# Kernel tuning notes

Hardware: AMD Instinct MI355X
Metric: run time of the kernel (lower is better)

Reference implementation:

```python
import jax, jax.numpy as jnp
import numpy as np

D_MODEL = 1024
HEADS = 16
HEAD_DIM = D_MODEL // HEADS


def setup_inputs() -> dict:
    key = jax.random.key(0)
    ks = jax.random.split(key, 9)
    s = 1.0 / np.sqrt(D_MODEL)
    inp = {
        "inputs": jax.random.normal(ks[0], (4, 2048, D_MODEL), dtype=jnp.float32),
        "Wq": jax.random.normal(ks[1], (D_MODEL, D_MODEL), dtype=jnp.float32) * s,
        "bq": jnp.zeros((D_MODEL,), dtype=jnp.float32),
        "Wk": jax.random.normal(ks[2], (D_MODEL, D_MODEL), dtype=jnp.float32) * s,
        "bk": jnp.zeros((D_MODEL,), dtype=jnp.float32),
        "Wv": jax.random.normal(ks[3], (D_MODEL, D_MODEL), dtype=jnp.float32) * s,
        "bv": jnp.zeros((D_MODEL,), dtype=jnp.float32),
        "Wo": jax.random.normal(ks[4], (D_MODEL, D_MODEL), dtype=jnp.float32) * s,
        "bo": jnp.zeros((D_MODEL,), dtype=jnp.float32),
    }
    return inp


def reference(inputs, Wq, bq, Wk, bk, Wv, bv, Wo, bo):
    bs, seq, _ = inputs.shape
    # projections -> [b, h, s, d]
    def split_heads(x):
        return x.reshape(bs, seq, HEADS, HEAD_DIM).transpose(0, 2, 1, 3)
    q = split_heads(inputs @ Wq + bq)
    k = split_heads(inputs @ Wk + bk)
    v = split_heads(inputs @ Wv + bv)
    # NOTE: original code divides by (head_dim ** 1 / 2) == head_dim/2, not sqrt(head_dim)
    scale = HEAD_DIM / 2.0
    scores = jnp.einsum("bhqd,bhkd->bhqk", q, k) / scale
    attn = jax.nn.softmax(scores, axis=-1)
    out = jnp.einsum("bhqk,bhkd->bhqd", attn, v)
    out = out.transpose(0, 2, 1, 3).reshape(bs, seq, HEADS * HEAD_DIM)
    return out @ Wo + bo
```

## Files before the change

kernel.cpp:

```cpp
#include <hip/hip_runtime.h>
#include <stdint.h>

typedef __attribute__((ext_vector_type(8))) short bf16x8;
typedef __attribute__((ext_vector_type(4))) float f32x4;
typedef __attribute__((address_space(1))) void as1_void;
typedef __attribute__((address_space(3))) void as3_void;

#define D_MODEL 1024
#define SEQ     2048
#define BATCH   4
#define HEADS   16
#define HDIM    64

#define QSCALE 0.045084220029218407f

__device__ __forceinline__ ushort f2bf(float f) {
  union { float f; unsigned u; } v; v.f = f;
  unsigned u = v.u + 0x7fffu + ((v.u >> 16) & 1u);
  return (ushort)(u >> 16);
}

__device__ __forceinline__ void gload_lds16(const void* g, void* l) {
  __builtin_amdgcn_global_load_lds((as1_void*)(uintptr_t)g, (as3_void*)l, 16, 0, 0);
}

__device__ __forceinline__ bf16x8 pack8(float a0, float a1, float a2, float a3,
                                        float a4, float a5, float a6, float a7) {
  union { uint u[4]; bf16x8 v; } x;
  x.u[0] = __builtin_amdgcn_perm(__float_as_uint(a1), __float_as_uint(a0), 0x07060302);
  x.u[1] = __builtin_amdgcn_perm(__float_as_uint(a3), __float_as_uint(a2), 0x07060302);
  x.u[2] = __builtin_amdgcn_perm(__float_as_uint(a5), __float_as_uint(a4), 0x07060302);
  x.u[3] = __builtin_amdgcn_perm(__float_as_uint(a7), __float_as_uint(a6), 0x07060302);
  return x.v;
}

__global__ void prep_kernel(const float* __restrict__ X,
                            const float* w0, const float* w1, const float* w2, const float* w3,
                            const float* __restrict__ bq, const float* __restrict__ bk,
                            const float* __restrict__ bv,
                            ushort* __restrict__ Xb, ushort* __restrict__ WT,
                            float* __restrict__ bcat) {
  __shared__ float tile[32][33];
  const int bx = blockIdx.x, t = threadIdx.x;
  if (bx < 8192) {
    int i = bx * 256 + t;
    float4 f = reinterpret_cast<const float4*>(X)[i];
    ushort4 o;
    o.x = f2bf(f.x); o.y = f2bf(f.y); o.z = f2bf(f.z); o.w = f2bf(f.w);
    reinterpret_cast<ushort4*>(Xb)[i] = o;
  } else if (bx < 12288) {
    int tz = bx - 8192;
    int z = tz >> 10;
    int xy = tz & 1023;
    int bxt = xy & 31, byt = xy >> 5;
    const float* w = (z == 0) ? w0 : (z == 1) ? w1 : (z == 2) ? w2 : w3;
    const float sc = (z == 0) ? QSCALE : 1.0f;
    ushort* o = WT + (size_t)z * D_MODEL * D_MODEL;
    int tx = t & 31, ty = t >> 5;
    int x = bxt * 32 + tx;
    int y0 = byt * 32;
    #pragma unroll
    for (int i = ty; i < 32; i += 8)
      tile[i][tx] = w[(size_t)(y0 + i) * D_MODEL + x];
    __syncthreads();
    #pragma unroll
    for (int i = ty; i < 32; i += 8)
      o[(size_t)(bxt * 32 + i) * D_MODEL + y0 + tx] = f2bf(tile[tx][i] * sc);
  } else {
    int i = (bx - 12288) * 256 + t;
    bcat[i] = (i < 1024) ? bq[i] * QSCALE : (i < 2048) ? bk[i - 1024] : bv[i - 2048];
  }
}

__global__ __launch_bounds__(256) void gemm_qkv(const ushort* __restrict__ A, const ushort* __restrict__ BT,
                                                const float* __restrict__ bias,
                                                ushort* __restrict__ QK, ushort* __restrict__ Vt) {
  __shared__ __align__(16) ushort As[128 * 32];
  __shared__ __align__(16) ushort Bs[128 * 32];
  const int K = D_MODEL;
  const int tid  = threadIdx.x;
  const int w    = tid >> 6;
  const int lane = tid & 63;
  const int lo   = lane & 15, quad = lane >> 4;
  const int m0 = blockIdx.y * 128, n0 = blockIdx.x * 128;
  const int ra = lane >> 2;
  const int ca = (lane & 3) * 8;
  const int wm = (w & 1) * 64, wn = (w >> 1) * 64;

  f32x4 acc[4][4];
  #pragma unroll
  for (int i = 0; i < 4; ++i)
    #pragma unroll
    for (int j = 0; j < 4; ++j) acc[i][j] = {0.f, 0.f, 0.f, 0.f};

  for (int k0 = 0; k0 < K; k0 += 32) {
    #pragma unroll
    for (int i = 0; i < 2; ++i) {
      const int j = w * 2 + i;
      gload_lds16(A  + (size_t)(m0 + j * 16 + ra) * K + k0 + ca, &As[j * 512]);
      gload_lds16(BT + (size_t)(n0 + j * 16 + ra) * K + k0 + ca, &Bs[j * 512]);
    }
    __syncthreads();
    bf16x8 af[4], bfv[4];
    #pragma unroll
    for (int mi = 0; mi < 4; ++mi) af[mi]  = *(const bf16x8*)&As[(wm + mi * 16 + lo) * 32 + quad * 8];
    #pragma unroll
    for (int ni = 0; ni < 4; ++ni) bfv[ni] = *(const bf16x8*)&Bs[(wn + ni * 16 + lo) * 32 + quad * 8];
    #pragma unroll
    for (int mi = 0; mi < 4; ++mi)
      #pragma unroll
      for (int ni = 0; ni < 4; ++ni)
        acc[mi][ni] = __builtin_amdgcn_mfma_f32_16x16x32_bf16(af[mi], bfv[ni], acc[mi][ni], 0, 0, 0);
    __syncthreads();
  }

  if (blockIdx.x < 16) {
    #pragma unroll
    for (int ni = 0; ni < 4; ++ni) {
      const int col = n0 + wn + ni * 16 + lo;
      const float bv = bias[col];
      #pragma unroll
      for (int mi = 0; mi < 4; ++mi) {
        #pragma unroll
        for (int r = 0; r < 4; ++r) {
          const int row = m0 + wm + mi * 16 + quad * 4 + r;
          QK[(size_t)row * 2048 + col] = f2bf(acc[mi][ni][r] + bv);
        }
      }
    }
  } else {
    #pragma unroll
    for (int ni = 0; ni < 4; ++ni) {
      const int col  = n0 + wn + ni * 16 + lo;
      const int vcol = col - 2048;
      const int hh = vcol >> 6, d = vcol & 63;
      const float bv = bias[col];
      #pragma unroll
      for (int mi = 0; mi < 4; ++mi) {
        const int base = m0 + wm + mi * 16;
        const int brow = base + quad * 4;
        const int bidx = brow >> 11;
        const int srow = brow & 2047;
        const int ck   = srow >> 6;
        const int c0   = (base & 32) + (quad << 3) + ((base >> 2) & 4);
        ushort e0 = f2bf(acc[mi][ni][0] + bv);
        ushort e1 = f2bf(acc[mi][ni][1] + bv);
        ushort e2 = f2bf(acc[mi][ni][2] + bv);
        ushort e3 = f2bf(acc[mi][ni][3] + bv);
        uint2 pk;
        pk.x = (uint)e0 | ((uint)e1 << 16);
        pk.y = (uint)e2 | ((uint)e3 << 16);
        *(uint2*)&Vt[(size_t)((bidx * HEADS + hh) * HDIM + d) * SEQ + ck * 64 + c0] = pk;
      }
    }
  }
}

__global__ __launch_bounds__(256) void gemm_bt_f32(const ushort* __restrict__ A, const ushort* __restrict__ BT,
                                                   const float* __restrict__ bias, float* __restrict__ C,
                                                   int M, int N, int K) {
  __shared__ __align__(16) ushort As[128 * 32];
  __shared__ __align__(16) ushort Bs[128 * 32];
  const int tid  = threadIdx.x;
  const int w    = tid >> 6;
  const int lane = tid & 63;
  const int lo   = lane & 15, quad = lane >> 4;
  const int m0 = blockIdx.y * 128, n0 = blockIdx.x * 128;
  const int ra = lane >> 2;
  const int ca = (lane & 3) * 8;
  const int wm = (w & 1) * 64, wn = (w >> 1) * 64;

  f32x4 acc[4][4];
  #pragma unroll
  for (int i = 0; i < 4; ++i)
    #pragma unroll
    for (int j = 0; j < 4; ++j) acc[i][j] = {0.f, 0.f, 0.f, 0.f};

  for (int k0 = 0; k0 < K; k0 += 32) {
    #pragma unroll
    for (int i = 0; i < 2; ++i) {
      const int j = w * 2 + i;
      gload_lds16(A  + (size_t)(m0 + j * 16 + ra) * K + k0 + ca, &As[j * 512]);
      gload_lds16(BT + (size_t)(n0 + j * 16 + ra) * K + k0 + ca, &Bs[j * 512]);
    }
    __syncthreads();
    bf16x8 af[4], bfv[4];
    #pragma unroll
    for (int mi = 0; mi < 4; ++mi) af[mi]  = *(const bf16x8*)&As[(wm + mi * 16 + lo) * 32 + quad * 8];
    #pragma unroll
    for (int ni = 0; ni < 4; ++ni) bfv[ni] = *(const bf16x8*)&Bs[(wn + ni * 16 + lo) * 32 + quad * 8];
    #pragma unroll
    for (int mi = 0; mi < 4; ++mi)
      #pragma unroll
      for (int ni = 0; ni < 4; ++ni)
        acc[mi][ni] = __builtin_amdgcn_mfma_f32_16x16x32_bf16(af[mi], bfv[ni], acc[mi][ni], 0, 0, 0);
    __syncthreads();
  }

  #pragma unroll
  for (int ni = 0; ni < 4; ++ni) {
    const int col = n0 + wn + ni * 16 + lo;
    const float bv = bias[col];
    #pragma unroll
    for (int mi = 0; mi < 4; ++mi) {
      #pragma unroll
      for (int r = 0; r < 4; ++r) {
        const int row = m0 + wm + mi * 16 + quad * 4 + r;
        C[(size_t)row * N + col] = acc[mi][ni][r] + bv;
      }
    }
  }
}

__global__ __launch_bounds__(256, 2) void attn_kernel(const ushort* __restrict__ QK,
                                                      const ushort* __restrict__ Vt,
                                                      ushort* __restrict__ Og) {
  __shared__ __align__(16) ushort Ks[64 * 64];
  __shared__ __align__(16) ushort Vs[64 * 64];

  const int tid  = threadIdx.x;
  const int w    = tid >> 6, lane = tid & 63;
  const int lo   = lane & 15, quad = lane >> 4;
  const int h = blockIdx.y, b = blockIdx.z;
  const int qbase = blockIdx.x * 256 + w * 64;
  const int swz = lo & 7;

  bf16x8 qf[4][2];
  #pragma unroll
  for (int qg = 0; qg < 4; ++qg) {
    const ushort* qp = QK + (size_t)(b * SEQ + qbase + qg * 16 + lo) * 2048 + h * HDIM;
    qf[qg][0] = *(const bf16x8*)(qp + quad * 8);
    qf[qg][1] = *(const bf16x8*)(qp + 32 + quad * 8);
  }

  f32x4 acc[4][4];
  #pragma unroll
  for (int qg = 0; qg < 4; ++qg)
    #pragma unroll
    for (int t = 0; t < 4; ++t) acc[qg][t] = {0.f, 0.f, 0.f, 0.f};
  float lsum[4] = {0.f, 0.f, 0.f, 0.f};

  for (int ck = 0; ck < SEQ / 64; ++ck) {
    __syncthreads();
    #pragma unroll
    for (int i = 0; i < 2; ++i) {
      const int c16 = (w * 2 + i) * 64 + lane;
      const int r = c16 >> 3, ps = c16 & 7;
      const int gs = ps ^ (r & 7);
      gload_lds16(QK + (size_t)(b * SEQ + ck * 64 + r) * 2048 + 1024 + h * HDIM + gs * 8,
                  &Ks[(w * 2 + i) * 512]);
      gload_lds16(Vt + (size_t)((b * HEADS + h) * HDIM + r) * SEQ + ck * 64 + gs * 8,
                  &Vs[(w * 2 + i) * 512]);
    }
    __syncthreads();

    bf16x8 kf[4][2];
    #pragma unroll
    for (int sub = 0; sub < 4; ++sub) {
      const ushort* kr = &Ks[(sub * 16 + lo) * 64];
      kf[sub][0] = *(const bf16x8*)(kr + ((quad ^ swz) * 8));
      kf[sub][1] = *(const bf16x8*)(kr + (((4 + quad) ^ swz) * 8));
    }

    bf16x8 af[4][2];
    #pragma unroll
    for (int qg = 0; qg < 4; ++qg) {
      f32x4 s[4];
      #pragma unroll
      for (int sub = 0; sub < 4; ++sub) s[sub] = {0.f, 0.f, 0.f, 0.f};
      #pragma unroll
      for (int sub = 0; sub < 4; ++sub) {
        s[sub] = __builtin_amdgcn_mfma_f32_16x16x32_bf16(kf[sub][0], qf[qg][0], s[sub], 0, 0, 0);
        s[sub] = __builtin_amdgcn_mfma_f32_16x16x32_bf16(kf[sub][1], qf[qg][1], s[sub], 0, 0, 0);
      }
      float p[4][4];
      #pragma unroll
      for (int sub = 0; sub < 4; ++sub)
        #pragma unroll
        for (int r = 0; r < 4; ++r) p[sub][r] = __builtin_amdgcn_exp2f(s[sub][r]);
      float t0 = 0.f;
      #pragma unroll
      for (int sub = 0; sub < 4; ++sub)
        t0 += (p[sub][0] + p[sub][1]) + (p[sub][2] + p[sub][3]);
      lsum[qg] += t0;
      af[qg][0] = pack8(p[0][0], p[0][1], p[0][2], p[0][3], p[1][0], p[1][1], p[1][2], p[1][3]);
      af[qg][1] = pack8(p[2][0], p[2][1], p[2][2], p[2][3], p[3][0], p[3][1], p[3][2], p[3][3]);
    }

    #pragma unroll
    for (int t = 0; t < 4; ++t) {
      const ushort* vr = &Vs[(t * 16 + lo) * 64];
      #pragma unroll
      for (int hh = 0; hh < 2; ++hh) {
        bf16x8 vf = *(const bf16x8*)(vr + (((hh * 4 + quad) ^ swz) * 8));
        #pragma unroll
        for (int qg = 0; qg < 4; ++qg)
          acc[qg][t] = __builtin_amdgcn_mfma_f32_16x16x32_bf16(af[qg][hh], vf, acc[qg][t], 0, 0, 0);
      }
    }
  }

  #pragma unroll
  for (int qg = 0; qg < 4; ++qg) {
    float v = lsum[qg];
    v += __shfl_xor(v, 16);
    v += __shfl_xor(v, 32);
    float linv[4];
    #pragma unroll
    for (int r = 0; r < 4; ++r) linv[r] = 1.0f / __shfl(v, quad * 4 + r);
    #pragma unroll
    for (int t = 0; t < 4; ++t)
      #pragma unroll
      for (int r = 0; r < 4; ++r)
        Og[(size_t)(b * SEQ + qbase + qg * 16 + quad * 4 + r) * D_MODEL + h * HDIM + t * 16 + lo] =
            f2bf(acc[qg][t][r] * linv[r]);
  }
}

extern "C" void kernel_launch(void* const* d_in, const int* in_sizes, int n_in,
                              void* d_out, int out_size, void* d_ws, size_t ws_size,
                              hipStream_t stream) {
  const float* X  = (const float*)d_in[0];
  const float* Wq = (const float*)d_in[1];
  const float* bq = (const float*)d_in[2];
  const float* Wk = (const float*)d_in[3];
  const float* bk = (const float*)d_in[4];
  const float* Wv = (const float*)d_in[5];
  const float* bv = (const float*)d_in[6];
  const float* Wo = (const float*)d_in[7];
  const float* bo = (const float*)d_in[8];
  float* out = (float*)d_out;
  char* ws = (char*)d_ws;

  ushort* Xb  = (ushort*)(ws);
  ushort* WT  = (ushort*)(ws + 16777216);
  ushort* QKb = (ushort*)(ws + 25165824);
  ushort* Vtb = (ushort*)(ws + 58720256);
  ushort* Ob  = (ushort*)(ws + 75497472);
  float*  bcat = (float*)(ws + 75497472);
  const int WSTRIDE = D_MODEL * D_MODEL;

  prep_kernel<<<12300, 256, 0, stream>>>(X, Wq, Wk, Wv, Wo, bq, bk, bv, Xb, WT, bcat);

  gemm_qkv<<<dim3(24, 64), 256, 0, stream>>>(Xb, WT, bcat, QKb, Vtb);

  attn_kernel<<<dim3(SEQ / 256, HEADS, BATCH), 256, 0, stream>>>(QKb, Vtb, Ob);

  gemm_bt_f32<<<dim3(8, 64), 256, 0, stream>>>(Ob, WT + 3 * WSTRIDE, bo, out,
                                               BATCH * SEQ, D_MODEL, D_MODEL);
}
```

Baseline: 276.9 us.

## Rewrite QKV GEMM as 256x256 double-buffered pipelined kernel with swizzled LDS

```diff
diff --git a/kernel.cpp b/kernel.cpp
--- a/kernel.cpp
+++ b/kernel.cpp
@@ -72,72 +72,188 @@
   }
 }
 
-__global__ __launch_bounds__(256) void gemm_qkv(const ushort* __restrict__ A, const ushort* __restrict__ BT,
-                                                const float* __restrict__ bias,
-                                                ushort* __restrict__ QK, ushort* __restrict__ Vt) {
-  __shared__ __align__(16) ushort As[128 * 32];
-  __shared__ __align__(16) ushort Bs[128 * 32];
-  const int K = D_MODEL;
+#define MFMA16(a, b, c) __builtin_amdgcn_mfma_f32_16x16x32_bf16(a, b, c, 0, 0, 0)
+
+__global__ __launch_bounds__(512, 2) void gemm_qkv(const ushort* __restrict__ A, const ushort* __restrict__ BT,
+                                                   const float* __restrict__ bias,
+                                                   ushort* __restrict__ QK, ushort* __restrict__ Vt) {
+  __shared__ __align__(16) char smem[131072];
   const int tid  = threadIdx.x;
   const int w    = tid >> 6;
   const int lane = tid & 63;
   const int lo   = lane & 15, quad = lane >> 4;
-  const int m0 = blockIdx.y * 128, n0 = blockIdx.x * 128;
-  const int ra = lane >> 2;
-  const int ca = (lane & 3) * 8;
-  const int wm = (w & 1) * 64, wn = (w >> 1) * 64;
-
-  f32x4 acc[4][4];
-  #pragma unroll
-  for (int i = 0; i < 4; ++i)
+  const int wr   = w >> 2, wc = w & 3;
+
+  const int orig = blockIdx.y * 12 + blockIdx.x;
+  const int wg   = (orig & 7) * 48 + (orig >> 3);
+  const int m0   = (wg / 12) * 256;
+  const int n0   = (wg % 12) * 256;
+
+  const int tl = tid ^ (((tid >> 5) & 1) << 1);
+  const ushort* sA = A  + (size_t)(m0 + (tl >> 3)) * 1024 + (tl & 7) * 8;
+  const ushort* sB = BT + (size_t)(n0 + (tl >> 3)) * 1024 + (tl & 7) * 8;
+  char* lw = smem + w * 1024;
+
+  const int rdq = (quad * 16) ^ ((lo & 4) << 3);
+  const int rdA = wr * 16384 + lo * 128 + rdq;
+  const int rdB = 65536 + (wc * 64 + lo) * 128 + rdq;
+
+  f32x4 acc[8][4];
+  #pragma unroll
+  for (int i = 0; i < 8; ++i)
     #pragma unroll
     for (int j = 0; j < 4; ++j) acc[i][j] = {0.f, 0.f, 0.f, 0.f};
 
-  for (int k0 = 0; k0 < K; k0 += 32) {
-    #pragma unroll
-    for (int i = 0; i < 2; ++i) {
-      const int j = w * 2 + i;
-      gload_lds16(A  + (size_t)(m0 + j * 16 + ra) * K + k0 + ca, &As[j * 512]);
-      gload_lds16(BT + (size_t)(n0 + j * 16 + ra) * K + k0 + ca, &Bs[j * 512]);
-    }
-    __syncthreads();
-    bf16x8 af[4], bfv[4];
-    #pragma unroll
-    for (int mi = 0; mi < 4; ++mi) af[mi]  = *(const bf16x8*)&As[(wm + mi * 16 + lo) * 32 + quad * 8];
-    #pragma unroll
-    for (int ni = 0; ni < 4; ++ni) bfv[ni] = *(const bf16x8*)&Bs[(wn + ni * 16 + lo) * 32 + quad * 8];
-    #pragma unroll
-    for (int mi = 0; mi < 4; ++mi)
-      #pragma unroll
-      for (int ni = 0; ni < 4; ++ni)
-        acc[mi][ni] = __builtin_amdgcn_mfma_f32_16x16x32_bf16(af[mi], bfv[ni], acc[mi][ni], 0, 0, 0);
-    __syncthreads();
-  }
-
-  if (blockIdx.x < 16) {
+  gload_lds16(sB,              lw + 65536);
+  gload_lds16(sB +  64 * 1024, lw + 65536 +  8192);
+  gload_lds16(sB + 128 * 1024, lw + 65536 + 16384);
+  gload_lds16(sB + 192 * 1024, lw + 65536 + 24576);
+  gload_lds16(sA,              lw);
+  gload_lds16(sA + 128 * 1024, lw + 16384);
+  gload_lds16(sA +  64 * 1024, lw +  8192);
+  gload_lds16(sA + 192 * 1024, lw + 24576);
+  asm volatile("s_waitcnt vmcnt(2)" ::: "memory");
+  __builtin_amdgcn_s_barrier();
+  asm volatile("" ::: "memory");
+
+  const char* L = smem;
+  #pragma unroll 2
+  for (int kt = 0; kt < 16; ++kt) {
+    const int b32 = (kt & 1) << 15;
+    const int nb  = b32 ^ 32768;
+    const int kc  = (kt + 1) * 64;
+    const bool pf = kt < 15;
+    bf16x8 bfr[4][2], af0[2], af1[2];
+
+    #pragma unroll
+    for (int ni = 0; ni < 4; ++ni)
+      #pragma unroll
+      for (int ks = 0; ks < 2; ++ks)
+        bfr[ni][ks] = *(const bf16x8*)(L + b32 + rdB + ni * 2048 + ks * 64);
+    #pragma unroll
+    for (int ks = 0; ks < 2; ++ks) {
+      af0[ks] = *(const bf16x8*)(L + b32 + rdA + ks * 64);
+      af1[ks] = *(const bf16x8*)(L + b32 + rdA + 2048 + ks * 64);
+    }
+    if (pf) {
+      gload_lds16(sB + kc,             lw + nb + 65536);
+      gload_lds16(sB + 64 * 1024 + kc, lw + nb + 65536 + 8192);
+    }
+    asm volatile("s_waitcnt lgkmcnt(8)" ::: "memory");
+    __builtin_amdgcn_s_barrier();
+    asm volatile("s_waitcnt lgkmcnt(0)" ::: "memory");
+    __builtin_amdgcn_sched_barrier(0);
+    __builtin_amdgcn_s_setprio(1);
+    #pragma unroll
+    for (int ks = 0; ks < 2; ++ks)
+      #pragma unroll
+      for (int ni = 0; ni < 4; ++ni) {
+        acc[0][ni] = MFMA16(af0[ks], bfr[ni][ks], acc[0][ni]);
+        acc[1][ni] = MFMA16(af1[ks], bfr[ni][ks], acc[1][ni]);
+      }
+    __builtin_amdgcn_s_setprio(0);
+    __builtin_amdgcn_s_barrier();
+    asm volatile("" ::: "memory");
+
+    #pragma unroll
+    for (int ks = 0; ks < 2; ++ks) {
+      af0[ks] = *(const bf16x8*)(L + b32 + rdA + 2 * 2048 + ks * 64);
+      af1[ks] = *(const bf16x8*)(L + b32 + rdA + 3 * 2048 + ks * 64);
+    }
+    if (pf) {
+      gload_lds16(sB + 128 * 1024 + kc, lw + nb + 65536 + 16384);
+      gload_lds16(sB + 192 * 1024 + kc, lw + nb + 65536 + 24576);
+    }
+    __builtin_amdgcn_s_barrier();
+    asm volatile("s_waitcnt lgkmcnt(0)" ::: "memory");
+    __builtin_amdgcn_sched_barrier(0);
+    __builtin_amdgcn_s_setprio(1);
+    #pragma unroll
+    for (int ks = 0; ks < 2; ++ks)
+      #pragma unroll
+      for (int ni = 0; ni < 4; ++ni) {
+        acc[2][ni] = MFMA16(af0[ks], bfr[ni][ks], acc[2][ni]);
+        acc[3][ni] = MFMA16(af1[ks], bfr[ni][ks], acc[3][ni]);
+      }
+    __builtin_amdgcn_s_setprio(0);
+    if (pf) asm volatile("s_waitcnt vmcnt(4)" ::: "memory");
+    else    asm volatile("s_waitcnt vmcnt(0)" ::: "memory");
+    __builtin_amdgcn_s_barrier();
+    asm volatile("" ::: "memory");
+
+    #pragma unroll
+    for (int ks = 0; ks < 2; ++ks) {
+      af0[ks] = *(const bf16x8*)(L + b32 + rdA + 4 * 2048 + ks * 64);
+      af1[ks] = *(const bf16x8*)(L + b32 + rdA + 5 * 2048 + ks * 64);
+    }
+    if (pf) {
+      gload_lds16(sA + kc,              lw + nb);
+      gload_lds16(sA + 128 * 1024 + kc, lw + nb + 16384);
+    }
+    __builtin_amdgcn_s_barrier();
+    asm volatile("s_waitcnt lgkmcnt(0)" ::: "memory");
+    __builtin_amdgcn_sched_barrier(0);
+    __builtin_amdgcn_s_setprio(1);
+    #pragma unroll
+    for (int ks = 0; ks < 2; ++ks)
+      #pragma unroll
+      for (int ni = 0; ni < 4; ++ni) {
+        acc[4][ni] = MFMA16(af0[ks], bfr[ni][ks], acc[4][ni]);
+        acc[5][ni] = MFMA16(af1[ks], bfr[ni][ks], acc[5][ni]);
+      }
+    __builtin_amdgcn_s_setprio(0);
+    __builtin_amdgcn_s_barrier();
+    asm volatile("" ::: "memory");
+
+    #pragma unroll
+    for (int ks = 0; ks < 2; ++ks) {
+      af0[ks] = *(const bf16x8*)(L + b32 + rdA + 6 * 2048 + ks * 64);
+      af1[ks] = *(const bf16x8*)(L + b32 + rdA + 7 * 2048 + ks * 64);
+    }
+    if (pf) {
+      gload_lds16(sA + 64 * 1024 + kc,  lw + nb + 8192);
+      gload_lds16(sA + 192 * 1024 + kc, lw + nb + 24576);
+    }
+    __builtin_amdgcn_s_barrier();
+    asm volatile("s_waitcnt lgkmcnt(0)" ::: "memory");
+    __builtin_amdgcn_sched_barrier(0);
+    __builtin_amdgcn_s_setprio(1);
+    #pragma unroll
+    for (int ks = 0; ks < 2; ++ks)
+      #pragma unroll
+      for (int ni = 0; ni < 4; ++ni) {
+        acc[6][ni] = MFMA16(af0[ks], bfr[ni][ks], acc[6][ni]);
+        acc[7][ni] = MFMA16(af1[ks], bfr[ni][ks], acc[7][ni]);
+      }
+    __builtin_amdgcn_s_setprio(0);
+    if (pf) asm volatile("s_waitcnt vmcnt(2)" ::: "memory");
+    __builtin_amdgcn_s_barrier();
+    asm volatile("" ::: "memory");
+  }
+
+  if (n0 < 2048) {
     #pragma unroll
     for (int ni = 0; ni < 4; ++ni) {
-      const int col = n0 + wn + ni * 16 + lo;
+      const int col = n0 + wc * 64 + ni * 16 + lo;
       const float bv = bias[col];
       #pragma unroll
-      for (int mi = 0; mi < 4; ++mi) {
+      for (int mi = 0; mi < 8; ++mi) {
+        const int row = m0 + wr * 128 + mi * 16 + quad * 4;
         #pragma unroll
-        for (int r = 0; r < 4; ++r) {
-          const int row = m0 + wm + mi * 16 + quad * 4 + r;
-          QK[(size_t)row * 2048 + col] = f2bf(acc[mi][ni][r] + bv);
-        }
+        for (int r = 0; r < 4; ++r)
+          QK[(size_t)(row + r) * 2048 + col] = f2bf(acc[mi][ni][r] + bv);
       }
     }
   } else {
     #pragma unroll
     for (int ni = 0; ni < 4; ++ni) {
-      const int col  = n0 + wn + ni * 16 + lo;
+      const int col  = n0 + wc * 64 + ni * 16 + lo;
       const int vcol = col - 2048;
       const int hh = vcol >> 6, d = vcol & 63;
       const float bv = bias[col];
       #pragma unroll
-      for (int mi = 0; mi < 4; ++mi) {
-        const int base = m0 + wm + mi * 16;
+      for (int mi = 0; mi < 8; ++mi) {
+        const int base = m0 + wr * 128 + mi * 16;
         const int brow = base + quad * 4;
         const int bidx = brow >> 11;
         const int srow = brow & 2047;
@@ -342,7 +458,7 @@
 
   prep_kernel<<<12300, 256, 0, stream>>>(X, Wq, Wk, Wv, Wo, bq, bk, bv, Xb, WT, bcat);
 
-  gemm_qkv<<<dim3(24, 64), 256, 0, stream>>>(Xb, WT, bcat, QKb, Vtb);
+  gemm_qkv<<<dim3(12, 32), 512, 0, stream>>>(Xb, WT, bcat, QKb, Vtb);
 
   attn_kernel<<<dim3(SEQ / 256, HEADS, BATCH), 256, 0, stream>>>(QKb, Vtb, Ob);
 
```

New measurement: 272.3 us. About the same (-1.7%).
